# Performance work log

Measured on AMD Instinct MI355X. Metric: run time of the kernel, lower is better.

## Reference

```python
import jax, jax.numpy as jnp
import numpy as np

B, DIM, N, RATIO, K, EPS = 32, 512, 2048, 8, 6, 2e-08
R = DIM // RATIO  # 64


def setup_inputs() -> dict:
    key = jax.random.key(0)
    k1, k2, k3 = jax.random.split(key, 3)
    x = jax.random.normal(k1, (B, DIM, N), dtype=jnp.float32)
    D = jax.random.uniform(k2, (DIM, R), dtype=jnp.float32)  # uniform(0,1) init like torch
    C = jax.random.uniform(k3, (R, N), dtype=jnp.float32)
    return {"x": x, "D": D, "C": C}


def _step(x, D, C, eps):
    # x: [b, d, n], D: [b, d, r], C: [b, r, n]
    Dt = jnp.swapaxes(D, -1, -2)  # [b, r, d]
    Ct = jnp.swapaxes(C, -1, -2)  # [b, n, r]
    C_new = C * ((Dt @ x) / (Dt @ D @ C + eps))
    D_new = D * ((x @ Ct) / (D @ C @ Ct + eps))
    return D_new, C_new


def reference(x, D, C):
    b = x.shape[0]
    x = jax.nn.relu(x)
    Db = jnp.broadcast_to(D, (b,) + D.shape)  # repeat 'd r -> b d r'
    Cb = jnp.broadcast_to(C, (b,) + C.shape)  # repeat 'r n -> b r n'
    D_, C_ = Db, Cb
    for k in reversed(range(K)):
        if k > 0:
            # torch runs these iterations under no_grad -> detach outputs
            D_, C_ = jax.lax.stop_gradient(_step(x, D_, C_, EPS))
        else:
            D_, C_ = _step(x, D_, C_, EPS)
    return D_ @ C_  # [b, d, n]
```

## Files before the change

### kernel.cpp

```cpp
#include <hip/hip_runtime.h>

#define B_ 32
#define DIM_ 512
#define N_ 2048
#define R_ 64
#define K_ 6
#define EPS_ 2e-8f

typedef short bf16x8 __attribute__((ext_vector_type(8)));
typedef float f32x4 __attribute__((ext_vector_type(4)));

__device__ __forceinline__ unsigned short f2bf(float f) {
  unsigned u = __float_as_uint(f);
  unsigned r = (u + 0x7FFFu + ((u >> 16) & 1u)) >> 16;
  return (unsigned short)r;
}
__device__ __forceinline__ float bf2f(unsigned short h) {
  return __uint_as_float(((unsigned)h) << 16);
}

__global__ __launch_bounds__(256) void k_xprep(const float* __restrict__ x, short* __restrict__ xbf,
                                               short* __restrict__ xbt) {
  const int b = blockIdx.z, d0 = blockIdx.y * 64, n0 = blockIdx.x * 64;
  const int t = threadIdx.x;
  __shared__ float tile[64 * 65];
  const float* xg = x + (size_t)b * DIM_ * N_ + (size_t)d0 * N_ + n0;
  short* xn = xbf + (size_t)b * DIM_ * N_ + (size_t)d0 * N_ + n0;
#pragma unroll
  for (int i = 0; i < 2; ++i) {
    int idx = i * 256 + t;
    int d = idx >> 3, c = idx & 7;
    float4 a = *(const float4*)(xg + (size_t)d * N_ + c * 8);
    float4 e = *(const float4*)(xg + (size_t)d * N_ + c * 8 + 4);
    unsigned h[8];
    h[0] = f2bf(fmaxf(a.x, 0.f)); h[1] = f2bf(fmaxf(a.y, 0.f));
    h[2] = f2bf(fmaxf(a.z, 0.f)); h[3] = f2bf(fmaxf(a.w, 0.f));
    h[4] = f2bf(fmaxf(e.x, 0.f)); h[5] = f2bf(fmaxf(e.y, 0.f));
    h[6] = f2bf(fmaxf(e.z, 0.f)); h[7] = f2bf(fmaxf(e.w, 0.f));
    unsigned o[4];
#pragma unroll
    for (int k = 0; k < 4; ++k) o[k] = h[2 * k] | (h[2 * k + 1] << 16);
    *(int4*)(xn + (size_t)d * N_ + c * 8) = *(const int4*)o;
#pragma unroll
    for (int j = 0; j < 8; ++j) tile[d * 65 + c * 8 + j] = __uint_as_float(h[j] << 16);
  }
  __syncthreads();
  short* xt = xbt + (size_t)b * N_ * DIM_ + (size_t)n0 * DIM_ + d0;
#pragma unroll
  for (int i = 0; i < 2; ++i) {
    int idx = i * 256 + t;
    int n = idx >> 3, c = idx & 7;
    unsigned o[4];
#pragma unroll
    for (int k = 0; k < 4; ++k) {
      unsigned lo = __float_as_uint(tile[(c * 8 + 2 * k) * 65 + n]);
      unsigned hi = __float_as_uint(tile[(c * 8 + 2 * k + 1) * 65 + n]);
      o[k] = (lo >> 16) | (hi & 0xFFFF0000u);
    }
    *(int4*)(xt + (size_t)n * DIM_ + c * 8) = *(const int4*)o;
  }
}

__global__ __launch_bounds__(256) void k_bcastD(const float* __restrict__ D, float* __restrict__ Db,
                                                short* __restrict__ Dbf, short* __restrict__ Dbt,
                                                float* __restrict__ DtDp) {
  const int b = blockIdx.y, d0 = blockIdx.x * 64, t = threadIdx.x;
  const int w = t >> 6, ln = t & 15, lg = (t & 63) >> 4;
  __shared__ short dtt[64 * 72];
#pragma unroll
  for (int j = 0; j < 16; ++j) {
    int idx = t + j * 256;
    int d = idx >> 6, r = idx & 63;
    float v = D[(size_t)(d0 + d) * R_ + r];
    Db[((size_t)b * DIM_ + d0 + d) * R_ + r] = v;
    unsigned short h = f2bf(v);
    Dbf[((size_t)b * DIM_ + d0 + d) * R_ + r] = (short)h;
    dtt[r * 72 + d] = (short)h;
  }
  __syncthreads();
#pragma unroll
  for (int j = 0; j < 2; ++j) {
    int i = t + j * 256;
    int row = i >> 3, c = i & 7;
    *(int4*)(Dbt + ((size_t)b * R_ + row) * DIM_ + d0 + c * 8) = *(const int4*)(dtt + row * 72 + c * 8);
  }
  f32x4 g[4];
#pragma unroll
  for (int nt = 0; nt < 4; ++nt) g[nt] = (f32x4){0.f, 0.f, 0.f, 0.f};
#pragma unroll
  for (int kc = 0; kc < 2; ++kc) {
    bf16x8 a = *(const bf16x8*)(dtt + (w * 16 + ln) * 72 + kc * 32 + lg * 8);
#pragma unroll
    for (int nt = 0; nt < 4; ++nt) {
      bf16x8 bb = *(const bf16x8*)(dtt + (nt * 16 + ln) * 72 + kc * 32 + lg * 8);
      g[nt] = __builtin_amdgcn_mfma_f32_16x16x32_bf16(a, bb, g[nt], 0, 0, 0);
    }
  }
  float* Po = DtDp + ((size_t)b * 8 + blockIdx.x) * 4096;
#pragma unroll
  for (int nt = 0; nt < 4; ++nt)
#pragma unroll
    for (int q = 0; q < 4; ++q) Po[(w * 16 + lg * 4 + q) * 64 + nt * 16 + ln] = g[nt][q];
}

__global__ __launch_bounds__(256) void k_bcastC(const float* __restrict__ C,
                                                short* __restrict__ Cbf, short* __restrict__ Cbt,
                                                float* __restrict__ CCtp) {
  const int b = blockIdx.y, ns = blockIdx.x * 128, t = threadIdx.x;
  const int w = t >> 6, ln = t & 15, lg = (t & 63) >> 4;
  __shared__ short crt[64 * 136];
  __shared__ short ctt[128 * 72];
#pragma unroll
  for (int j = 0; j < 32; ++j) {
    int idx = t + j * 256;
    int r = idx >> 7, n = idx & 127;
    float v = C[(size_t)r * N_ + ns + n];
    unsigned short h = f2bf(v);
    Cbf[((size_t)b * R_ + r) * N_ + ns + n] = (short)h;
    crt[r * 136 + n] = (short)h;
    ctt[n * 72 + r] = (short)h;
  }
  __syncthreads();
#pragma unroll
  for (int j = 0; j < 4; ++j) {
    int i = t + j * 256;
    int row = i >> 3, c = i & 7;
    *(int4*)(Cbt + ((size_t)b * N_ + ns + row) * R_ + c * 8) = *(const int4*)(ctt + row * 72 + c * 8);
  }
  f32x4 g[4];
#pragma unroll
  for (int nt = 0; nt < 4; ++nt) g[nt] = (f32x4){0.f, 0.f, 0.f, 0.f};
#pragma unroll
  for (int kc = 0; kc < 4; ++kc) {
    bf16x8 a = *(const bf16x8*)(crt + (w * 16 + ln) * 136 + kc * 32 + lg * 8);
#pragma unroll
    for (int nt = 0; nt < 4; ++nt) {
      bf16x8 bb = *(const bf16x8*)(crt + (nt * 16 + ln) * 136 + kc * 32 + lg * 8);
      g[nt] = __builtin_amdgcn_mfma_f32_16x16x32_bf16(a, bb, g[nt], 0, 0, 0);
    }
  }
  float* Po = CCtp + ((size_t)b * 16 + blockIdx.x) * 4096;
#pragma unroll
  for (int nt = 0; nt < 4; ++nt)
#pragma unroll
    for (int q = 0; q < 4; ++q) Po[(w * 16 + lg * 4 + q) * 64 + nt * 16 + ln] = g[nt][q];
}

__global__ __launch_bounds__(256) void k_gram(const float* __restrict__ DtDp, const float* __restrict__ CCtp,
                                              short* __restrict__ dtdF, short* __restrict__ cctF) {
  const int b = blockIdx.x, t = threadIdx.x;
  {
    const float4* P = (const float4*)(DtDp + (size_t)b * 8 * 4096);
#pragma unroll
    for (int j = 0; j < 4; ++j) {
      int idx4 = t + j * 256;
      float4 a = P[idx4];
#pragma unroll
      for (int ss = 1; ss < 8; ++ss) {
        float4 v = P[ss * 1024 + idx4];
        a.x += v.x; a.y += v.y; a.z += v.z; a.w += v.w;
      }
      unsigned o0 = (unsigned)f2bf(a.x) | ((unsigned)f2bf(a.y) << 16);
      unsigned o1 = (unsigned)f2bf(a.z) | ((unsigned)f2bf(a.w) << 16);
      *(uint2*)(dtdF + (size_t)b * 4096 + idx4 * 4) = make_uint2(o0, o1);
    }
  }
  {
    const float4* P = (const float4*)(CCtp + (size_t)b * 16 * 4096);
#pragma unroll
    for (int j = 0; j < 4; ++j) {
      int idx4 = t + j * 256;
      float4 a = P[idx4];
#pragma unroll
      for (int ss = 1; ss < 16; ++ss) {
        float4 v = P[ss * 1024 + idx4];
        a.x += v.x; a.y += v.y; a.z += v.z; a.w += v.w;
      }
      unsigned o0 = (unsigned)f2bf(a.x) | ((unsigned)f2bf(a.y) << 16);
      unsigned o1 = (unsigned)f2bf(a.z) | ((unsigned)f2bf(a.w) << 16);
      *(uint2*)(cctF + (size_t)b * 4096 + idx4 * 4) = make_uint2(o0, o1);
    }
  }
}

template <bool LAST>
__global__ __launch_bounds__(256, 2) void k_AC(
    const short* __restrict__ xbt, const short* __restrict__ Dbt_o,
    const short* __restrict__ Cbt_o, const short* __restrict__ dtdF,
    short* __restrict__ Cbf_n, short* __restrict__ Cbt_n, float* __restrict__ CCtp_n) {
  const int f = blockIdx.x;
  const int b = f & 31, nt_i = f >> 5;
  const int ns = nt_i * 128;
  const int t = threadIdx.x;
  const int w = t >> 6, ln = t & 15, lg = (t & 63) >> 4;
  __shared__ __align__(16) char smem[55296];
  short* xs0 = (short*)smem;
  short* xs1 = (short*)(smem + 18432);
  short* ds0 = (short*)(smem + 36864);
  short* ds1 = (short*)(smem + 46080);
  short* dtd = (short*)smem;
  short* crt = (short*)(smem + 9216);
  short* ctt = (short*)(smem + 26624);

  const short* xg = xbt + ((size_t)b * N_ + ns) * DIM_;
  const short* dg = Dbt_o + (size_t)b * R_ * DIM_;
  int4 xv[4], dv[2];

#define LOADX(kc)                                                                       \
  {                                                                                     \
    _Pragma("unroll") for (int j = 0; j < 4; ++j) {                                     \
      int idx = j * 256 + t;                                                            \
      xv[j] = *(const int4*)(xg + (size_t)(idx >> 3) * DIM_ + (kc) * 64 + (idx & 7) * 8); \
    }                                                                                   \
    _Pragma("unroll") for (int j = 0; j < 2; ++j) {                                     \
      int idx = j * 256 + t;                                                            \
      dv[j] = *(const int4*)(dg + (size_t)(idx >> 3) * DIM_ + (kc) * 64 + (idx & 7) * 8); \
    }                                                                                   \
  }
#define STOREX(xs, ds)                                                  \
  {                                                                     \
    _Pragma("unroll") for (int j = 0; j < 4; ++j) {                     \
      int idx = j * 256 + t;                                            \
      *(int4*)((xs) + (idx >> 3) * 72 + (idx & 7) * 8) = xv[j];         \
    }                                                                   \
    _Pragma("unroll") for (int j = 0; j < 2; ++j) {                     \
      int idx = j * 256 + t;                                            \
      *(int4*)((ds) + (idx >> 3) * 72 + (idx & 7) * 8) = dv[j];         \
    }                                                                   \
  }

  f32x4 acc[4][2];
#pragma unroll
  for (int mt = 0; mt < 4; ++mt)
#pragma unroll
    for (int nt = 0; nt < 2; ++nt) acc[mt][nt] = (f32x4){0.f, 0.f, 0.f, 0.f};

  LOADX(0);
  STOREX(xs0, ds0);
  __syncthreads();
  for (int kc = 0; kc < 8; ++kc) {
    if (kc < 7) LOADX(kc + 1);
    short* xs = (kc & 1) ? xs1 : xs0;
    short* ds = (kc & 1) ? ds1 : ds0;
#pragma unroll
    for (int kk = 0; kk < 2; ++kk) {
      bf16x8 af[4], bfv[2];
#pragma unroll
      for (int mt = 0; mt < 4; ++mt) af[mt] = *(const bf16x8*)(ds + (mt * 16 + ln) * 72 + kk * 32 + lg * 8);
#pragma unroll
      for (int nt = 0; nt < 2; ++nt)
        bfv[nt] = *(const bf16x8*)(xs + (w * 32 + nt * 16 + ln) * 72 + kk * 32 + lg * 8);
#pragma unroll
      for (int mt = 0; mt < 4; ++mt)
#pragma unroll
        for (int nt = 0; nt < 2; ++nt)
          acc[mt][nt] = __builtin_amdgcn_mfma_f32_16x16x32_bf16(af[mt], bfv[nt], acc[mt][nt], 0, 0, 0);
    }
    if (kc < 7) {
      short* xsn = (kc & 1) ? xs0 : xs1;
      short* dsn = (kc & 1) ? ds0 : ds1;
      STOREX(xsn, dsn);
    }
    __syncthreads();
  }
#undef LOADX
#undef STOREX

  {
    const short* G = dtdF + (size_t)b * 4096;
#pragma unroll
    for (int j = 0; j < 2; ++j) {
      int i = t + j * 256;
      *(int4*)(dtd + (i >> 3) * 72 + (i & 7) * 8) = *(const int4*)(G + i * 8);
    }
  }
  __syncthreads();
  f32x4 accd[4][2];
#pragma unroll
  for (int mt = 0; mt < 4; ++mt)
#pragma unroll
    for (int nt = 0; nt < 2; ++nt) accd[mt][nt] = (f32x4){0.f, 0.f, 0.f, 0.f};
#pragma unroll
  for (int kc2 = 0; kc2 < 2; ++kc2) {
    bf16x8 cb[2], am[4];
#pragma unroll
    for (int nt = 0; nt < 2; ++nt)
      cb[nt] = *(const bf16x8*)(Cbt_o + ((size_t)b * N_ + ns + w * 32 + nt * 16 + ln) * R_ + kc2 * 32 + lg * 8);
#pragma unroll
    for (int mt = 0; mt < 4; ++mt) am[mt] = *(const bf16x8*)(dtd + (mt * 16 + ln) * 72 + kc2 * 32 + lg * 8);
#pragma unroll
    for (int mt = 0; mt < 4; ++mt)
#pragma unroll
      for (int nt = 0; nt < 2; ++nt)
        accd[mt][nt] = __builtin_amdgcn_mfma_f32_16x16x32_bf16(am[mt], cb[nt], accd[mt][nt], 0, 0, 0);
  }
#pragma unroll
  for (int mt = 0; mt < 4; ++mt)
#pragma unroll
    for (int nt = 0; nt < 2; ++nt) {
      int n = w * 32 + nt * 16 + ln;
      ushort4 cv = *(const ushort4*)(Cbt_o + ((size_t)b * N_ + ns + n) * R_ + mt * 16 + lg * 4);
      unsigned short cvv[4] = {cv.x, cv.y, cv.z, cv.w};
#pragma unroll
      for (int q = 0; q < 4; ++q) {
        int r = mt * 16 + lg * 4 + q;
        float co = bf2f(cvv[q]);
        float cn = co * acc[mt][nt][q] / (accd[mt][nt][q] + EPS_);
        unsigned short h = f2bf(cn);
        crt[r * 136 + n] = (short)h;
        ctt[n * 72 + r] = (short)h;
      }
    }
  __syncthreads();
  if constexpr (!LAST) {
#pragma unroll
    for (int j = 0; j < 4; ++j) {
      int i = t + j * 256;
      int row = i >> 4, c = i & 15;
      *(int4*)(Cbf_n + ((size_t)b * R_ + row) * N_ + ns + c * 8) = *(const int4*)(crt + row * 136 + c * 8);
    }
  }
#pragma unroll
  for (int j = 0; j < 4; ++j) {
    int i = t + j * 256;
    int row = i >> 3, c = i & 7;
    *(int4*)(Cbt_n + ((size_t)b * N_ + ns + row) * R_ + c * 8) = *(const int4*)(ctt + row * 72 + c * 8);
  }
  if constexpr (!LAST) {
    f32x4 g[4];
#pragma unroll
    for (int nt = 0; nt < 4; ++nt) g[nt] = (f32x4){0.f, 0.f, 0.f, 0.f};
#pragma unroll
    for (int kc3 = 0; kc3 < 4; ++kc3) {
      bf16x8 a = *(const bf16x8*)(crt + (w * 16 + ln) * 136 + kc3 * 32 + lg * 8);
#pragma unroll
      for (int nt2 = 0; nt2 < 4; ++nt2) {
        bf16x8 bb = *(const bf16x8*)(crt + (nt2 * 16 + ln) * 136 + kc3 * 32 + lg * 8);
        g[nt2] = __builtin_amdgcn_mfma_f32_16x16x32_bf16(a, bb, g[nt2], 0, 0, 0);
      }
    }
    float* Po = CCtp_n + ((size_t)b * 16 + nt_i) * 4096;
#pragma unroll
    for (int nt2 = 0; nt2 < 4; ++nt2)
#pragma unroll
      for (int q = 0; q < 4; ++q) Po[(w * 16 + lg * 4 + q) * 64 + nt2 * 16 + ln] = g[nt2][q];
  }
}

template <bool LAST>
__global__ __launch_bounds__(512, 2) void k_XD(
    const short* __restrict__ xbf, const short* __restrict__ Cbf_o, const float* __restrict__ Db_o,
    const short* __restrict__ Dbf_o, const short* __restrict__ cctF, float* __restrict__ Db_n,
    short* __restrict__ Dbf_n, short* __restrict__ Dbt_n, float* __restrict__ DtDp_n) {
  const int f = blockIdx.x;
  const int b = f & 31, dt_i = f >> 5;
  const int d0 = dt_i * 64;
  const int t = threadIdx.x;
  const int w = t >> 6, ln = t & 15, lg = (t & 63) >> 4;
  const int kh = w >> 2, wq = w & 3;
  __shared__ __align__(16) char smem[73728];
  float* red = (float*)smem;
  short* cct = (short*)(smem + 16384);
  short* dtt = (short*)(smem + 25600);

  const int tsel = t >> 7, tt = t & 127;
  const short* gsrc = (tsel & 1) ? (Cbf_o + (size_t)b * R_ * N_) : (xbf + ((size_t)b * DIM_ + d0) * N_);
  const int nbase = (tsel >> 1) * 1024;
  int4 v[4];

#define LOADV(kc)                                                                         \
  {                                                                                       \
    _Pragma("unroll") for (int j = 0; j < 4; ++j) {                                       \
      int idx = j * 128 + tt;                                                             \
      v[j] = *(const int4*)(gsrc + (size_t)(idx >> 3) * N_ + nbase + (kc) * 64 + (idx & 7) * 8); \
    }                                                                                     \
  }
#define STOREV(pb)                                                                  \
  {                                                                                 \
    short* dst = (short*)(smem + ((pb) * 4 + tsel) * 9216);                         \
    _Pragma("unroll") for (int j = 0; j < 4; ++j) {                                 \
      int idx = j * 128 + tt;                                                       \
      *(int4*)(dst + (idx >> 3) * 72 + (idx & 7) * 8) = v[j];                       \
    }                                                                               \
  }

  f32x4 acc[4];
#pragma unroll
  for (int nt = 0; nt < 4; ++nt) acc[nt] = (f32x4){0.f, 0.f, 0.f, 0.f};

  LOADV(0);
  STOREV(0);
  __syncthreads();
  for (int cc = 0; cc < 16; ++cc) {
    if (cc < 15) LOADV(cc + 1);
    const int p = cc & 1;
    short* sx = (short*)(smem + (p * 4 + kh * 2) * 9216);
    short* sc = (short*)(smem + (p * 4 + kh * 2 + 1) * 9216);
#pragma unroll
    for (int kk = 0; kk < 2; ++kk) {
      bf16x8 a = *(const bf16x8*)(sx + (wq * 16 + ln) * 72 + kk * 32 + lg * 8);
#pragma unroll
      for (int nt = 0; nt < 4; ++nt) {
        bf16x8 bb = *(const bf16x8*)(sc + (nt * 16 + ln) * 72 + kk * 32 + lg * 8);
        acc[nt] = __builtin_amdgcn_mfma_f32_16x16x32_bf16(a, bb, acc[nt], 0, 0, 0);
      }
    }
    if (cc < 15) STOREV((cc + 1) & 1);
    __syncthreads();
  }
#undef LOADV
#undef STOREV

  if (kh == 1) {
#pragma unroll
    for (int nt = 0; nt < 4; ++nt)
#pragma unroll
      for (int q = 0; q < 4; ++q) red[(wq * 16 + nt * 4 + q) * 64 + (t & 63)] = acc[nt][q];
  }
  {
    const short* G = cctF + (size_t)b * 4096;
    *(int4*)(cct + (t >> 3) * 72 + (t & 7) * 8) = *(const int4*)(G + t * 8);
  }
  __syncthreads();
  if (kh == 0) {
#pragma unroll
    for (int nt = 0; nt < 4; ++nt)
#pragma unroll
      for (int q = 0; q < 4; ++q) acc[nt][q] += red[(wq * 16 + nt * 4 + q) * 64 + (t & 63)];
    f32x4 accd[4];
#pragma unroll
    for (int nt = 0; nt < 4; ++nt) accd[nt] = (f32x4){0.f, 0.f, 0.f, 0.f};
#pragma unroll
    for (int kc = 0; kc < 2; ++kc) {
      bf16x8 a = *(const bf16x8*)(Dbf_o + ((size_t)b * DIM_ + d0 + wq * 16 + ln) * R_ + kc * 32 + lg * 8);
#pragma unroll
      for (int nt = 0; nt < 4; ++nt) {
        bf16x8 bb = *(const bf16x8*)(cct + (nt * 16 + ln) * 72 + kc * 32 + lg * 8);
        accd[nt] = __builtin_amdgcn_mfma_f32_16x16x32_bf16(a, bb, accd[nt], 0, 0, 0);
      }
    }
#pragma unroll
    for (int nt = 0; nt < 4; ++nt)
#pragma unroll
      for (int q = 0; q < 4; ++q) {
        int dl = wq * 16 + lg * 4 + q;
        int r = nt * 16 + ln;
        size_t gi = ((size_t)b * DIM_ + d0 + dl) * R_ + r;
        float dold = Db_o[gi];
        float dn = dold * acc[nt][q] / (accd[nt][q] + EPS_);
        unsigned short h = f2bf(dn);
        Dbf_n[gi] = (short)h;
        if constexpr (!LAST) {
          Db_n[gi] = dn;
          dtt[r * 72 + dl] = (short)h;
        }
      }
  }
  __syncthreads();
  if constexpr (!LAST) {
    if (t < 512) {
      int row = t >> 3, c = t & 7;
      *(int4*)(Dbt_n + ((size_t)b * R_ + row) * DIM_ + d0 + c * 8) = *(const int4*)(dtt + row * 72 + c * 8);
    }
    if (kh == 0) {
      f32x4 g[4];
#pragma unroll
      for (int nt = 0; nt < 4; ++nt) g[nt] = (f32x4){0.f, 0.f, 0.f, 0.f};
#pragma unroll
      for (int kc = 0; kc < 2; ++kc) {
        bf16x8 a = *(const bf16x8*)(dtt + (wq * 16 + ln) * 72 + kc * 32 + lg * 8);
#pragma unroll
        for (int nt2 = 0; nt2 < 4; ++nt2) {
          bf16x8 bb = *(const bf16x8*)(dtt + (nt2 * 16 + ln) * 72 + kc * 32 + lg * 8);
          g[nt2] = __builtin_amdgcn_mfma_f32_16x16x32_bf16(a, bb, g[nt2], 0, 0, 0);
        }
      }
      float* Po = DtDp_n + ((size_t)b * 8 + dt_i) * 4096;
#pragma unroll
      for (int nt2 = 0; nt2 < 4; ++nt2)
#pragma unroll
        for (int q = 0; q < 4; ++q) Po[(wq * 16 + lg * 4 + q) * 64 + nt2 * 16 + ln] = g[nt2][q];
    }
  }
}

__global__ __launch_bounds__(256) void k_out(const short* __restrict__ Dbf, const short* __restrict__ Cbt,
                                             float* __restrict__ out) {
  const int b = blockIdx.z, d0 = blockIdx.y * 64, n0 = blockIdx.x * 128;
  const int t = threadIdx.x;
  const int w = t >> 6, ln = t & 15, lg = (t & 63) >> 4;
  __shared__ short ct[128 * 72];
  __shared__ short dn[64 * 72];
#pragma unroll
  for (int i = 0; i < 4; ++i) {
    int idx = i * 256 + t;
    int row = idx >> 3, c = idx & 7;
    *(int4*)(ct + row * 72 + c * 8) =
        *(const int4*)(Cbt + (size_t)b * N_ * R_ + (size_t)(n0 + row) * R_ + c * 8);
  }
#pragma unroll
  for (int i = 0; i < 2; ++i) {
    int idx = i * 256 + t;
    int row = idx >> 3, c = idx & 7;
    *(int4*)(dn + row * 72 + c * 8) =
        *(const int4*)(Dbf + (size_t)b * DIM_ * R_ + (size_t)(d0 + row) * R_ + c * 8);
  }
  __syncthreads();
  f32x4 acc[4][2];
#pragma unroll
  for (int mt = 0; mt < 4; ++mt)
#pragma unroll
    for (int nt = 0; nt < 2; ++nt) acc[mt][nt] = (f32x4){0.f, 0.f, 0.f, 0.f};
#pragma unroll
  for (int kc = 0; kc < 2; ++kc) {
    bf16x8 a[4], bb[2];
#pragma unroll
    for (int mt = 0; mt < 4; ++mt) a[mt] = *(const bf16x8*)(dn + (mt * 16 + ln) * 72 + kc * 32 + lg * 8);
#pragma unroll
    for (int nt = 0; nt < 2; ++nt)
      bb[nt] = *(const bf16x8*)(ct + (w * 32 + nt * 16 + ln) * 72 + kc * 32 + lg * 8);
#pragma unroll
    for (int mt = 0; mt < 4; ++mt)
#pragma unroll
      for (int nt = 0; nt < 2; ++nt)
        acc[mt][nt] = __builtin_amdgcn_mfma_f32_16x16x32_bf16(a[mt], bb[nt], acc[mt][nt], 0, 0, 0);
  }
  float* op = out + (size_t)b * DIM_ * N_;
#pragma unroll
  for (int mt = 0; mt < 4; ++mt)
#pragma unroll
    for (int nt = 0; nt < 2; ++nt) {
      int n = n0 + w * 32 + nt * 16 + ln;
#pragma unroll
      for (int q = 0; q < 4; ++q)
        op[(size_t)(d0 + mt * 16 + lg * 4 + q) * N_ + n] = acc[mt][nt][q];
    }
}

extern "C" void kernel_launch(void* const* d_in, const int* in_sizes, int n_in,
                              void* d_out, int out_size, void* d_ws, size_t ws_size,
                              hipStream_t stream) {
  const float* x = (const float*)d_in[0];
  const float* D = (const float*)d_in[1];
  const float* C = (const float*)d_in[2];
  float* out = (float*)d_out;

  char* wsb = (char*)d_ws;
  short* xbf   = (short*)(wsb);
  short* Cbf0  = (short*)(wsb + 67108864);
  short* Cbt0  = (short*)(wsb + 75497472);
  float* Db0   = (float*)(wsb + 83886080);
  short* Dbf0  = (short*)(wsb + 88080384);
  short* Dbt0  = (short*)(wsb + 90177536);
  float* DtDp0 = (float*)(wsb + 92274688);
  float* DtDp1 = (float*)(wsb + 96468992);
  short* dtdF  = (short*)(wsb + 100663296);
  short* cctF  = (short*)(wsb + 100925440);
  char* ob = (char*)d_out;
  short* xbt   = (short*)(ob);
  short* Cbf1  = (short*)(ob + 67108864);
  short* Cbt1  = (short*)(ob + 75497472);
  float* Db1   = (float*)(ob + 83886080);
  short* Dbf1  = (short*)(ob + 88080384);
  short* Dbt1  = (short*)(ob + 90177536);
  float* CCtp0 = (float*)(ob + 92274688);
  float* CCtp1 = (float*)(ob + 100663296);

  short* CbfS[2]  = {Cbf0, Cbf1};
  short* CbtS[2]  = {Cbt0, Cbt1};
  float* DbS[2]   = {Db0, Db1};
  short* DbfS[2]  = {Dbf0, Dbf1};
  short* DbtS[2]  = {Dbt0, Dbt1};
  float* DtDpS[2] = {DtDp0, DtDp1};
  float* CCtpS[2] = {CCtp0, CCtp1};

  k_xprep<<<dim3(N_ / 64, DIM_ / 64, B_), 256, 0, stream>>>(x, xbf, xbt);
  k_bcastD<<<dim3(8, B_), 256, 0, stream>>>(D, Db0, Dbf0, Dbt0, DtDp0);
  k_bcastC<<<dim3(16, B_), 256, 0, stream>>>(C, Cbf0, Cbt0, CCtp0);

  for (int k = 0; k < K_ - 1; ++k) {
    int p = k & 1, q = 1 - p;
    k_gram<<<dim3(B_), 256, 0, stream>>>(DtDpS[p], CCtpS[p], dtdF, cctF);
    k_AC<false><<<dim3(512), 256, 0, stream>>>(xbt, DbtS[p], CbtS[p], dtdF,
                                               CbfS[q], CbtS[q], CCtpS[q]);
    k_XD<false><<<dim3(256), 512, 0, stream>>>(xbf, CbfS[p], DbS[p], DbfS[p], cctF,
                                               DbS[q], DbfS[q], DbtS[q], DtDpS[q]);
  }
  {
    k_gram<<<dim3(B_), 256, 0, stream>>>(DtDpS[1], CCtpS[1], dtdF, cctF);
    k_AC<true><<<dim3(512), 256, 0, stream>>>(xbt, DbtS[1], CbtS[1], dtdF,
                                              CbfS[0], CbtS[0], CCtpS[0]);
    k_XD<true><<<dim3(256), 512, 0, stream>>>(xbf, CbfS[1], DbS[1], DbfS[1], cctF,
                                              DbS[0], DbfS[0], DbtS[0], DtDpS[0]);
  }
  k_out<<<dim3(N_ / 128, DIM_ / 64, B_), 256, 0, stream>>>(Dbf0, Cbt0, out);
}
```

Measured before the change: 352.4 us.

## Load small D/C operands directly from global, shrink LDS, widen k_gram grid

In k_AC and k_XD, the small shared operand (Dt tile or C tile) is no longer staged through double-buffered LDS; each wave reads its MFMA fragments directly from global memory, which should hit in cache. This roughly halves LDS use per block and raises the launch-bounds occupancy hints (3 blocks for k_AC, 6 for k_XD). k_gram is split into 256 blocks, each reducing a slice of the partial Gram matrices, instead of 32 blocks doing whole batches. The trade-off is more uncoalesced global/L2 fragment loads inside the inner loops, plus possible register pressure from the higher occupancy targets.

```diff
diff --git a/kernel.cpp b/kernel.cpp
--- a/kernel.cpp
+++ b/kernel.cpp
@@ -148,43 +148,37 @@
 
 __global__ __launch_bounds__(256) void k_gram(const float* __restrict__ DtDp, const float* __restrict__ CCtp,
                                               short* __restrict__ dtdF, short* __restrict__ cctF) {
-  const int b = blockIdx.x, t = threadIdx.x;
-  {
+  const int b = blockIdx.x >> 3, g = blockIdx.x & 7;
+  const int t = threadIdx.x;
+  if (t < 128) {
+    int idx4 = g * 128 + t;
     const float4* P = (const float4*)(DtDp + (size_t)b * 8 * 4096);
-#pragma unroll
-    for (int j = 0; j < 4; ++j) {
-      int idx4 = t + j * 256;
-      float4 a = P[idx4];
-#pragma unroll
-      for (int ss = 1; ss < 8; ++ss) {
-        float4 v = P[ss * 1024 + idx4];
-        a.x += v.x; a.y += v.y; a.z += v.z; a.w += v.w;
-      }
-      unsigned o0 = (unsigned)f2bf(a.x) | ((unsigned)f2bf(a.y) << 16);
-      unsigned o1 = (unsigned)f2bf(a.z) | ((unsigned)f2bf(a.w) << 16);
-      *(uint2*)(dtdF + (size_t)b * 4096 + idx4 * 4) = make_uint2(o0, o1);
-    }
-  }
-  {
+    float4 a = P[idx4];
+#pragma unroll
+    for (int ss = 1; ss < 8; ++ss) {
+      float4 v = P[ss * 1024 + idx4];
+      a.x += v.x; a.y += v.y; a.z += v.z; a.w += v.w;
+    }
+    unsigned o0 = (unsigned)f2bf(a.x) | ((unsigned)f2bf(a.y) << 16);
+    unsigned o1 = (unsigned)f2bf(a.z) | ((unsigned)f2bf(a.w) << 16);
+    *(uint2*)(dtdF + (size_t)b * 4096 + idx4 * 4) = make_uint2(o0, o1);
+  } else {
+    int idx4 = g * 128 + (t - 128);
     const float4* P = (const float4*)(CCtp + (size_t)b * 16 * 4096);
-#pragma unroll
-    for (int j = 0; j < 4; ++j) {
-      int idx4 = t + j * 256;
-      float4 a = P[idx4];
-#pragma unroll
-      for (int ss = 1; ss < 16; ++ss) {
-        float4 v = P[ss * 1024 + idx4];
-        a.x += v.x; a.y += v.y; a.z += v.z; a.w += v.w;
-      }
-      unsigned o0 = (unsigned)f2bf(a.x) | ((unsigned)f2bf(a.y) << 16);
-      unsigned o1 = (unsigned)f2bf(a.z) | ((unsigned)f2bf(a.w) << 16);
-      *(uint2*)(cctF + (size_t)b * 4096 + idx4 * 4) = make_uint2(o0, o1);
-    }
+    float4 a = P[idx4];
+#pragma unroll
+    for (int ss = 1; ss < 16; ++ss) {
+      float4 v = P[ss * 1024 + idx4];
+      a.x += v.x; a.y += v.y; a.z += v.z; a.w += v.w;
+    }
+    unsigned o0 = (unsigned)f2bf(a.x) | ((unsigned)f2bf(a.y) << 16);
+    unsigned o1 = (unsigned)f2bf(a.z) | ((unsigned)f2bf(a.w) << 16);
+    *(uint2*)(cctF + (size_t)b * 4096 + idx4 * 4) = make_uint2(o0, o1);
   }
 }
 
 template <bool LAST>
-__global__ __launch_bounds__(256, 2) void k_AC(
+__global__ __launch_bounds__(256, 3) void k_AC(
     const short* __restrict__ xbt, const short* __restrict__ Dbt_o,
     const short* __restrict__ Cbt_o, const short* __restrict__ dtdF,
     short* __restrict__ Cbf_n, short* __restrict__ Cbt_n, float* __restrict__ CCtp_n) {
@@ -193,18 +187,16 @@
   const int ns = nt_i * 128;
   const int t = threadIdx.x;
   const int w = t >> 6, ln = t & 15, lg = (t & 63) >> 4;
-  __shared__ __align__(16) char smem[55296];
+  __shared__ __align__(16) char smem[45056];
   short* xs0 = (short*)smem;
   short* xs1 = (short*)(smem + 18432);
-  short* ds0 = (short*)(smem + 36864);
-  short* ds1 = (short*)(smem + 46080);
   short* dtd = (short*)smem;
   short* crt = (short*)(smem + 9216);
   short* ctt = (short*)(smem + 26624);
 
   const short* xg = xbt + ((size_t)b * N_ + ns) * DIM_;
   const short* dg = Dbt_o + (size_t)b * R_ * DIM_;
-  int4 xv[4], dv[2];
+  int4 xv[4];
 
 #define LOADX(kc)                                                                       \
   {                                                                                     \
@@ -212,21 +204,13 @@
       int idx = j * 256 + t;                                                            \
       xv[j] = *(const int4*)(xg + (size_t)(idx >> 3) * DIM_ + (kc) * 64 + (idx & 7) * 8); \
     }                                                                                   \
-    _Pragma("unroll") for (int j = 0; j < 2; ++j) {                                     \
-      int idx = j * 256 + t;                                                            \
-      dv[j] = *(const int4*)(dg + (size_t)(idx >> 3) * DIM_ + (kc) * 64 + (idx & 7) * 8); \
-    }                                                                                   \
-  }
-#define STOREX(xs, ds)                                                  \
+  }
+#define STOREX(xs)                                                      \
   {                                                                     \
     _Pragma("unroll") for (int j = 0; j < 4; ++j) {                     \
       int idx = j * 256 + t;                                            \
       *(int4*)((xs) + (idx >> 3) * 72 + (idx & 7) * 8) = xv[j];         \
     }                                                                   \
-    _Pragma("unroll") for (int j = 0; j < 2; ++j) {                     \
-      int idx = j * 256 + t;                                            \
-      *(int4*)((ds) + (idx >> 3) * 72 + (idx & 7) * 8) = dv[j];         \
-    }                                                                   \
   }
 
   f32x4 acc[4][2];
@@ -236,17 +220,20 @@
     for (int nt = 0; nt < 2; ++nt) acc[mt][nt] = (f32x4){0.f, 0.f, 0.f, 0.f};
 
   LOADX(0);
-  STOREX(xs0, ds0);
+  STOREX(xs0);
   __syncthreads();
   for (int kc = 0; kc < 8; ++kc) {
     if (kc < 7) LOADX(kc + 1);
     short* xs = (kc & 1) ? xs1 : xs0;
-    short* ds = (kc & 1) ? ds1 : ds0;
+    bf16x8 af2[2][4];
+#pragma unroll
+    for (int kk = 0; kk < 2; ++kk)
+#pragma unroll
+      for (int mt = 0; mt < 4; ++mt)
+        af2[kk][mt] = *(const bf16x8*)(dg + (size_t)(mt * 16 + ln) * DIM_ + kc * 64 + kk * 32 + lg * 8);
 #pragma unroll
     for (int kk = 0; kk < 2; ++kk) {
-      bf16x8 af[4], bfv[2];
-#pragma unroll
-      for (int mt = 0; mt < 4; ++mt) af[mt] = *(const bf16x8*)(ds + (mt * 16 + ln) * 72 + kk * 32 + lg * 8);
+      bf16x8 bfv[2];
 #pragma unroll
       for (int nt = 0; nt < 2; ++nt)
         bfv[nt] = *(const bf16x8*)(xs + (w * 32 + nt * 16 + ln) * 72 + kk * 32 + lg * 8);
@@ -254,12 +241,11 @@
       for (int mt = 0; mt < 4; ++mt)
 #pragma unroll
         for (int nt = 0; nt < 2; ++nt)
-          acc[mt][nt] = __builtin_amdgcn_mfma_f32_16x16x32_bf16(af[mt], bfv[nt], acc[mt][nt], 0, 0, 0);
+          acc[mt][nt] = __builtin_amdgcn_mfma_f32_16x16x32_bf16(af2[kk][mt], bfv[nt], acc[mt][nt], 0, 0, 0);
     }
     if (kc < 7) {
       short* xsn = (kc & 1) ? xs0 : xs1;
-      short* dsn = (kc & 1) ? ds0 : ds1;
-      STOREX(xsn, dsn);
+      STOREX(xsn);
     }
     __syncthreads();
   }
@@ -348,7 +334,7 @@
 }
 
 template <bool LAST>
-__global__ __launch_bounds__(512, 2) void k_XD(
+__global__ __launch_bounds__(512, 6) void k_XD(
     const short* __restrict__ xbf, const short* __restrict__ Cbf_o, const float* __restrict__ Db_o,
     const short* __restrict__ Dbf_o, const short* __restrict__ cctF, float* __restrict__ Db_n,
     short* __restrict__ Dbf_n, short* __restrict__ Dbt_n, float* __restrict__ DtDp_n) {
@@ -358,32 +344,33 @@
   const int t = threadIdx.x;
   const int w = t >> 6, ln = t & 15, lg = (t & 63) >> 4;
   const int kh = w >> 2, wq = w & 3;
-  __shared__ __align__(16) char smem[73728];
+  __shared__ __align__(16) char smem[36864];
   float* red = (float*)smem;
   short* cct = (short*)(smem + 16384);
   short* dtt = (short*)(smem + 25600);
 
-  const int tsel = t >> 7, tt = t & 127;
-  const short* gsrc = (tsel & 1) ? (Cbf_o + (size_t)b * R_ * N_) : (xbf + ((size_t)b * DIM_ + d0) * N_);
-  const int nbase = (tsel >> 1) * 1024;
-  int4 v[4];
-
-#define LOADV(kc)                                                                         \
-  {                                                                                       \
-    _Pragma("unroll") for (int j = 0; j < 4; ++j) {                                       \
-      int idx = j * 128 + tt;                                                             \
+  const int tile = t >> 8, tt = t & 255;
+  const short* gsrc = xbf + ((size_t)b * DIM_ + d0) * N_;
+  const int nbase = tile * 1024;
+  int4 v[2];
+
+#define LOADV(kc)                                                                               \
+  {                                                                                             \
+    _Pragma("unroll") for (int j = 0; j < 2; ++j) {                                             \
+      int idx = j * 256 + tt;                                                                   \
       v[j] = *(const int4*)(gsrc + (size_t)(idx >> 3) * N_ + nbase + (kc) * 64 + (idx & 7) * 8); \
-    }                                                                                     \
+    }                                                                                           \
   }
 #define STOREV(pb)                                                                  \
   {                                                                                 \
-    short* dst = (short*)(smem + ((pb) * 4 + tsel) * 9216);                         \
-    _Pragma("unroll") for (int j = 0; j < 4; ++j) {                                 \
-      int idx = j * 128 + tt;                                                       \
+    short* dst = (short*)(smem + ((pb) * 2 + tile) * 9216);                         \
+    _Pragma("unroll") for (int j = 0; j < 2; ++j) {                                 \
+      int idx = j * 256 + tt;                                                       \
       *(int4*)(dst + (idx >> 3) * 72 + (idx & 7) * 8) = v[j];                       \
     }                                                                               \
   }
 
+  const short* cg = Cbf_o + (size_t)b * R_ * N_;
   f32x4 acc[4];
 #pragma unroll
   for (int nt = 0; nt < 4; ++nt) acc[nt] = (f32x4){0.f, 0.f, 0.f, 0.f};
@@ -394,16 +381,19 @@
   for (int cc = 0; cc < 16; ++cc) {
     if (cc < 15) LOADV(cc + 1);
     const int p = cc & 1;
-    short* sx = (short*)(smem + (p * 4 + kh * 2) * 9216);
-    short* sc = (short*)(smem + (p * 4 + kh * 2 + 1) * 9216);
+    short* sx = (short*)(smem + (p * 2 + kh) * 9216);
+    bf16x8 bb2[2][4];
+#pragma unroll
+    for (int kk = 0; kk < 2; ++kk)
+#pragma unroll
+      for (int nt = 0; nt < 4; ++nt)
+        bb2[kk][nt] = *(const bf16x8*)(cg + (size_t)(nt * 16 + ln) * N_ + kh * 1024 + cc * 64 + kk * 32 + lg * 8);
 #pragma unroll
     for (int kk = 0; kk < 2; ++kk) {
       bf16x8 a = *(const bf16x8*)(sx + (wq * 16 + ln) * 72 + kk * 32 + lg * 8);
 #pragma unroll
-      for (int nt = 0; nt < 4; ++nt) {
-        bf16x8 bb = *(const bf16x8*)(sc + (nt * 16 + ln) * 72 + kk * 32 + lg * 8);
-        acc[nt] = __builtin_amdgcn_mfma_f32_16x16x32_bf16(a, bb, acc[nt], 0, 0, 0);
-      }
+      for (int nt = 0; nt < 4; ++nt)
+        acc[nt] = __builtin_amdgcn_mfma_f32_16x16x32_bf16(a, bb2[kk][nt], acc[nt], 0, 0, 0);
     }
     if (cc < 15) STOREV((cc + 1) & 1);
     __syncthreads();
@@ -458,7 +448,7 @@
   }
   __syncthreads();
   if constexpr (!LAST) {
-    if (t < 512) {
+    {
       int row = t >> 3, c = t & 7;
       *(int4*)(Dbt_n + ((size_t)b * R_ + row) * DIM_ + d0 + c * 8) = *(const int4*)(dtt + row * 72 + c * 8);
     }
@@ -580,14 +570,14 @@
 
   for (int k = 0; k < K_ - 1; ++k) {
     int p = k & 1, q = 1 - p;
-    k_gram<<<dim3(B_), 256, 0, stream>>>(DtDpS[p], CCtpS[p], dtdF, cctF);
+    k_gram<<<dim3(256), 256, 0, stream>>>(DtDpS[p], CCtpS[p], dtdF, cctF);
     k_AC<false><<<dim3(512), 256, 0, stream>>>(xbt, DbtS[p], CbtS[p], dtdF,
                                                CbfS[q], CbtS[q], CCtpS[q]);
     k_XD<false><<<dim3(256), 512, 0, stream>>>(xbf, CbfS[p], DbS[p], DbfS[p], cctF,
                                                DbS[q], DbfS[q], DbtS[q], DtDpS[q]);
   }
   {
-    k_gram<<<dim3(B_), 256, 0, stream>>>(DtDpS[1], CCtpS[1], dtdF, cctF);
+    k_gram<<<dim3(256), 256, 0, stream>>>(DtDpS[1], CCtpS[1], dtdF, cctF);
     k_AC<true><<<dim3(512), 256, 0, stream>>>(xbt, DbtS[1], CbtS[1], dtdF,
                                               CbfS[0], CbtS[0], CCtpS[0]);
     k_XD<true><<<dim3(256), 512, 0, stream>>>(xbf, CbfS[1], DbS[1], DbfS[1], cctF,
```

Result: slower. 497.4 us (+41.1%).
